# Performance work log

Hardware: AMD Instinct MI355X
Metric: run time of the kernel (lower is better)

## Reference

```python
import jax, jax.numpy as jnp
import numpy as np

N_GROUPS = 4
N_LIMITED_GROUPS = 2
TOP_K = 2
ROUTE_SCALE = 1.0


def setup_inputs() -> dict:
    key = jax.random.key(0)
    k1, k2, k3, k4 = jax.random.split(key, 4)
    n_tokens, dim, n_experts = 65536, 4096, 16
    return {
        "x": jax.random.normal(k1, (n_tokens, dim), dtype=jnp.float32),
        "w1_weight": jax.random.normal(k2, (n_experts, dim), dtype=jnp.float32) * 0.02,
        "w1_bias": jax.random.normal(k3, (n_experts,), dtype=jnp.float32) * 0.02,
        "route_bias": jax.random.normal(k4, (n_experts,), dtype=jnp.float32) * 0.02,
    }


def reference(x, w1_weight, w1_bias, route_bias):
    # Linear scorer: [N, E]
    logits = x @ w1_weight.T + w1_bias
    # softmax in fp32 (score_func == 'softmax')
    scores = jax.nn.softmax(logits.astype(jnp.float32), axis=-1)
    # bias add (moe_use_bias=True); original_scores includes the bias
    scores = scores + route_bias
    original_scores = scores

    n = x.shape[0]
    # group masking: view [N, n_groups, experts_per_group]
    g = scores.reshape(n, N_GROUPS, -1)
    group_scores = g.max(axis=-1)  # amax path since bias is not None
    _, gidx = jax.lax.top_k(group_scores, N_LIMITED_GROUPS)  # [N, n_limited]
    keep = jnp.zeros((n, N_GROUPS), dtype=bool).at[
        jnp.arange(n)[:, None], gidx
    ].set(True)
    masked = jnp.where(keep[:, :, None], g, -jnp.inf).reshape(n, -1)

    # top-k over masked scores; gather values from original (unmasked-at-topk) scores
    _, indices = jax.lax.top_k(masked, TOP_K)  # [N, k]
    values = jnp.take_along_axis(original_scores, indices, axis=1) * ROUTE_SCALE
    return values.astype(x.dtype), indices
```

## Files before the change

### kernel.cpp

```cpp
#include <hip/hip_runtime.h>
#include <math.h>

constexpr int NE = 16;
constexpr int NG = 4;
#define MARGIN 1e-4

typedef __attribute__((ext_vector_type(8))) short bf16x8;
typedef __attribute__((ext_vector_type(4))) float f32x4;

__device__ __forceinline__ unsigned short f2bf_rne(float f) {
    unsigned u = __float_as_uint(f);
    unsigned r = (u + 0x7fffu + ((u >> 16) & 1u)) >> 16;
    return (unsigned short)r;
}

__global__ __launch_bounds__(256)
void w_prep_kernel(const float* __restrict__ w, float* __restrict__ wt,
                   unsigned short* __restrict__ whi, unsigned short* __restrict__ wlo,
                   int dim, int n) {
    int id = blockIdx.x * 256 + threadIdx.x;
    if (id < n) {
        int e = id / dim;
        int k = id - e * dim;
        float f = w[id];
        wt[(size_t)k * NE + e] = f;
        unsigned short h = f2bf_rne(f);
        float back = __uint_as_float(((unsigned)h) << 16);
        whi[id] = h;
        wlo[id] = f2bf_rne(f - back);
    }
}

struct RouteR { double v1, v2; int i1, i2; double mg, mo, ms; };

__device__ __forceinline__ RouteR route_epilogue(const double* tot,
                                                 const float* w1b,
                                                 const float* rbias)
{
    double logit[NE];
    double m = -INFINITY;
#pragma unroll
    for (int e = 0; e < NE; ++e) {
        logit[e] = tot[e] + (double)w1b[e];
        m = fmax(m, logit[e]);
    }
    double ssum = 0.0, p[NE];
#pragma unroll
    for (int e = 0; e < NE; ++e) { p[e] = exp(logit[e] - m); ssum += p[e]; }
    double inv = 1.0 / ssum, sc[NE];
#pragma unroll
    for (int e = 0; e < NE; ++e) sc[e] = p[e] * inv + (double)rbias[e];

    double gm[NG];
#pragma unroll
    for (int g = 0; g < NG; ++g) {
        double a = fmax(sc[g * 4 + 0], sc[g * 4 + 1]);
        double b = fmax(sc[g * 4 + 2], sc[g * 4 + 3]);
        gm[g] = fmax(a, b);
    }
    int g1 = 0;
#pragma unroll
    for (int g = 1; g < NG; ++g) if (gm[g] > gm[g1]) g1 = g;
    int g2 = (g1 == 0) ? 1 : 0;
#pragma unroll
    for (int g = 0; g < NG; ++g) if (g != g1 && gm[g] > gm[g2]) g2 = g;
    double gm3 = -INFINITY;
#pragma unroll
    for (int g = 0; g < NG; ++g)
        if (g != g1 && g != g2 && gm[g] > gm3) gm3 = gm[g];

    RouteR r;
    r.v1 = -INFINITY; r.i1 = 0;
#pragma unroll
    for (int e = 0; e < NE; ++e) {
        int g = e >> 2;
        bool keep = (g == g1) || (g == g2);
        if (keep && sc[e] > r.v1) { r.v1 = sc[e]; r.i1 = e; }
    }
    r.v2 = -INFINITY; r.i2 = 0;
#pragma unroll
    for (int e = 0; e < NE; ++e) {
        int g = e >> 2;
        bool keep = ((g == g1) || (g == g2)) && (e != r.i1);
        if (keep && sc[e] > r.v2) { r.v2 = sc[e]; r.i2 = e; }
    }
    double v3 = -INFINITY;
#pragma unroll
    for (int e = 0; e < NE; ++e) {
        int g = e >> 2;
        bool keep = ((g == g1) || (g == g2)) && (e != r.i1) && (e != r.i2);
        if (keep && sc[e] > v3) v3 = sc[e];
    }
    r.mg = gm[g2] - gm3;
    r.mo = r.v1 - r.v2;
    r.ms = r.v2 - v3;
    return r;
}

__global__ __launch_bounds__(256)
void k1_mfma(const float* __restrict__ x,
             const unsigned short* __restrict__ whi,
             const unsigned short* __restrict__ wlo,
             const float* __restrict__ w1b,
             const float* __restrict__ rbias,
             float* __restrict__ dout,
             int* __restrict__ fcount,
             int* __restrict__ flist,
             int n_tokens, int dim)
{
    __shared__ float scl[4][16][NE + 1];
    const int tid  = threadIdx.x;
    const int wid  = tid >> 6;
    const int lane = tid & 63;
    const int m    = lane & 15;
    const int kg   = lane >> 4;
    const long tok0 = (long)blockIdx.x * 64 + wid * 16;
    const int nst = dim / 32;

    const float* xp = x + (tok0 + m) * (size_t)dim + kg * 8;
    const unsigned short* whp = whi + (size_t)m * dim + kg * 8;
    const unsigned short* wlp = wlo + (size_t)m * dim + kg * 8;

    f32x4 acc = {0.f, 0.f, 0.f, 0.f};

    float4 xa = *(const float4*)(xp);
    float4 xb = *(const float4*)(xp + 4);
    bf16x8 wh = *(const bf16x8*)(whp);
    bf16x8 wl = *(const bf16x8*)(wlp);

    for (int c = 0; c < nst; ++c) {
        float4 nxa = xa, nxb = xb;
        bf16x8 nwh = wh, nwl = wl;
        if (c + 1 < nst) {
            const float* xn = xp + (size_t)(c + 1) * 32;
            nxa = *(const float4*)(xn);
            nxb = *(const float4*)(xn + 4);
            nwh = *(const bf16x8*)(whp + (size_t)(c + 1) * 32);
            nwl = *(const bf16x8*)(wlp + (size_t)(c + 1) * 32);
        }

        float xf[8] = {xa.x, xa.y, xa.z, xa.w, xb.x, xb.y, xb.z, xb.w};
        bf16x8 xhi, xlo;
#pragma unroll
        for (int j = 0; j < 8; ++j) {
            float f = xf[j];
            unsigned short h = f2bf_rne(f);
            float back = __uint_as_float(((unsigned)h) << 16);
            xhi[j] = (short)h;
            xlo[j] = (short)f2bf_rne(f - back);
        }

        acc = __builtin_amdgcn_mfma_f32_16x16x32_bf16(xhi, wh, acc, 0, 0, 0);
        acc = __builtin_amdgcn_mfma_f32_16x16x32_bf16(xlo, wh, acc, 0, 0, 0);
        acc = __builtin_amdgcn_mfma_f32_16x16x32_bf16(xhi, wl, acc, 0, 0, 0);

        xa = nxa; xb = nxb; wh = nwh; wl = nwl;
    }

#pragma unroll
    for (int j = 0; j < 4; ++j)
        scl[wid][kg * 4 + j][m] = acc[j];

    if (lane < 16) {
        double tot[NE];
#pragma unroll
        for (int e = 0; e < NE; ++e) tot[e] = (double)scl[wid][lane][e];
        RouteR r = route_epilogue(tot, w1b, rbias);
        long tok = tok0 + lane;

        double mmin = fmin(r.mg, fmin(r.mo, r.ms));
        if (mmin < MARGIN) {
            int idx = atomicAdd(fcount, 1);
            if (idx < n_tokens) flist[idx] = (int)tok;
        }
        float2 vv; vv.x = (float)r.v1; vv.y = (float)r.v2;
        *(float2*)(dout + tok * 2) = vv;
        float2 iv; iv.x = (float)r.i1; iv.y = (float)r.i2;
        *(float2*)(dout + (long)n_tokens * 2 + tok * 2) = iv;
    }
}

__global__ __launch_bounds__(256)
void k2_recheck(const float* __restrict__ x,
                const float* __restrict__ wt,
                const float* __restrict__ w1b,
                const float* __restrict__ rbias,
                float* __restrict__ dout,
                const int* __restrict__ fcount,
                const int* __restrict__ flist,
                int n_tokens, int dim)
{
    const int tid  = threadIdx.x;
    const int lane = tid & 63;
    const int wavesPerBlock = blockDim.x >> 6;
    const int wglobal = blockIdx.x * wavesPerBlock + (tid >> 6);
    const int nwaves  = gridDim.x * wavesPerBlock;
    int nf = *fcount;
    if (nf > n_tokens) nf = n_tokens;
    const int nq = dim / 256;

    for (int i = wglobal; i < nf; i += nwaves) {
        const int t = flist[i];
        const float* xr = x + (size_t)t * dim;

        double part[NE];
#pragma unroll
        for (int e = 0; e < NE; ++e) part[e] = 0.0;

        for (int q = 0; q < nq; ++q) {
            float4 xv = *(const float4*)(xr + q * 256 + lane * 4);
#pragma unroll
            for (int j = 0; j < 4; ++j) {
                int k = q * 256 + lane * 4 + j;
                double xd = (double)((const float*)&xv)[j];
                const float* wr = wt + (size_t)k * NE;
#pragma unroll
                for (int e = 0; e < NE; ++e)
                    part[e] = fma(xd, (double)wr[e], part[e]);
            }
        }

#pragma unroll
        for (int off = 1; off < 64; off <<= 1) {
#pragma unroll
            for (int e = 0; e < NE; ++e)
                part[e] += __shfl_xor(part[e], off, 64);
        }

        RouteR r = route_epilogue(part, w1b, rbias);
        if (lane == 0) {
            float2 vv; vv.x = (float)r.v1; vv.y = (float)r.v2;
            *(float2*)(dout + (long)t * 2) = vv;
            float2 iv; iv.x = (float)r.i1; iv.y = (float)r.i2;
            *(float2*)(dout + (long)n_tokens * 2 + (long)t * 2) = iv;
        }
    }
}

__global__ __launch_bounds__(256)
void router_fallback(const float* __restrict__ x,
                     const float* __restrict__ w1w,
                     const float* __restrict__ w1b,
                     const float* __restrict__ rbias,
                     float* __restrict__ dout,
                     int n_tokens, int dim)
{
    __shared__ double wbuf4[4][16][NE];
    const int tid  = threadIdx.x;
    const int uwid = __builtin_amdgcn_readfirstlane(tid >> 6);
    const int lane = tid & 63;
    const int slice = dim / 4;
    const int nst  = slice / 16;
    const long tokA = (long)blockIdx.x * 128 + lane;
    const long tokB = tokA + 64;
    const float* xA = x + tokA * (size_t)dim + (size_t)uwid * slice;
    const float* xB = x + tokB * (size_t)dim + (size_t)uwid * slice;

    double accA[NE], accB[NE];
#pragma unroll
    for (int e = 0; e < NE; ++e) { accA[e] = 0.0; accB[e] = 0.0; }

    float4 a0 = *(const float4*)(xA + 0), a1 = *(const float4*)(xA + 4);
    float4 a2 = *(const float4*)(xA + 8), a3 = *(const float4*)(xA + 12);
    float4 b0 = *(const float4*)(xB + 0), b1 = *(const float4*)(xB + 4);
    float4 b2 = *(const float4*)(xB + 8), b3 = *(const float4*)(xB + 12);
    float4 wreg;
    {
        const int i0 = lane * 4;
#pragma unroll
        for (int j = 0; j < 4; ++j) {
            int i = i0 + j;
            ((float*)&wreg)[j] = w1w[(size_t)(i & 15) * dim + uwid * slice + (i >> 4)];
        }
    }

    for (int c = 0; c < nst; ++c) {
        {
            double* dst = &wbuf4[uwid][0][0] + lane * 4;
            dst[0] = (double)wreg.x;  dst[1] = (double)wreg.y;
            dst[2] = (double)wreg.z;  dst[3] = (double)wreg.w;
        }
        float4 na0=a0,na1=a1,na2=a2,na3=a3,nb0=b0,nb1=b1,nb2=b2,nb3=b3;
        if (c + 1 < nst) {
            const float* pa = xA + (c + 1) * 16;
            const float* pb = xB + (c + 1) * 16;
            na0 = *(const float4*)(pa + 0);  na1 = *(const float4*)(pa + 4);
            na2 = *(const float4*)(pa + 8);  na3 = *(const float4*)(pa + 12);
            nb0 = *(const float4*)(pb + 0);  nb1 = *(const float4*)(pb + 4);
            nb2 = *(const float4*)(pb + 8);  nb3 = *(const float4*)(pb + 12);
            const int kb = uwid * slice + (c + 1) * 16;
            const int i0 = lane * 4;
#pragma unroll
            for (int j = 0; j < 4; ++j) {
                int i = i0 + j;
                ((float*)&wreg)[j] = w1w[(size_t)(i & 15) * dim + kb + (i >> 4)];
            }
        }
        float fa[16], fb[16];
        fa[0]=a0.x; fa[1]=a0.y; fa[2]=a0.z; fa[3]=a0.w;
        fa[4]=a1.x; fa[5]=a1.y; fa[6]=a1.z; fa[7]=a1.w;
        fa[8]=a2.x; fa[9]=a2.y; fa[10]=a2.z; fa[11]=a2.w;
        fa[12]=a3.x; fa[13]=a3.y; fa[14]=a3.z; fa[15]=a3.w;
        fb[0]=b0.x; fb[1]=b0.y; fb[2]=b0.z; fb[3]=b0.w;
        fb[4]=b1.x; fb[5]=b1.y; fb[6]=b1.z; fb[7]=b1.w;
        fb[8]=b2.x; fb[9]=b2.y; fb[10]=b2.z; fb[11]=b2.w;
        fb[12]=b3.x; fb[13]=b3.y; fb[14]=b3.z; fb[15]=b3.w;
#pragma unroll
        for (int kk = 0; kk < 16; ++kk) {
            double xa_ = (double)fa[kk];
            double xb_ = (double)fb[kk];
#pragma unroll
            for (int ep = 0; ep < NE / 2; ++ep) {
                double2 wv = *(const double2*)&wbuf4[uwid][kk][ep * 2];
                accA[ep*2+0] = fma(xa_, wv.x, accA[ep*2+0]);
                accA[ep*2+1] = fma(xa_, wv.y, accA[ep*2+1]);
                accB[ep*2+0] = fma(xb_, wv.x, accB[ep*2+0]);
                accB[ep*2+1] = fma(xb_, wv.y, accB[ep*2+1]);
            }
        }
        a0=na0; a1=na1; a2=na2; a3=na3;
        b0=nb0; b1=nb1; b2=nb2; b3=nb3;
    }

    __syncthreads();
    __shared__ double red[3][2][64][NE + 1];
    if (uwid != 0) {
#pragma unroll
        for (int e = 0; e < NE; ++e) {
            red[uwid - 1][0][lane][e] = accA[e];
            red[uwid - 1][1][lane][e] = accB[e];
        }
    }
    __syncthreads();
    if (uwid != 0) return;

#pragma unroll
    for (int t = 0; t < 2; ++t) {
        double tot[NE];
#pragma unroll
        for (int e = 0; e < NE; ++e) {
            double a = (t == 0) ? accA[e] : accB[e];
            tot[e] = ((a + red[0][t][lane][e]) + red[1][t][lane][e])
                     + red[2][t][lane][e];
        }
        RouteR r = route_epilogue(tot, w1b, rbias);
        long tok = (t == 0) ? tokA : tokB;
        float2 vv; vv.x = (float)r.v1; vv.y = (float)r.v2;
        *(float2*)(dout + tok * 2) = vv;
        float2 iv; iv.x = (float)r.i1; iv.y = (float)r.i2;
        *(float2*)(dout + (long)n_tokens * 2 + tok * 2) = iv;
    }
}

extern "C" void kernel_launch(void* const* d_in, const int* in_sizes, int n_in,
                              void* d_out, int out_size, void* d_ws, size_t ws_size,
                              hipStream_t stream)
{
    const float* x   = (const float*)d_in[0];
    const float* w1w = (const float*)d_in[1];
    const float* w1b = (const float*)d_in[2];
    const float* rb  = (const float*)d_in[3];
    float* out = (float*)d_out;

    const int ne       = in_sizes[2];
    const int dim      = in_sizes[1] / ne;
    const int n_tokens = in_sizes[0] / dim;

    const int nW = dim * ne;
    const size_t WT_BYTES  = (size_t)nW * sizeof(float);
    const size_t WHI_OFF   = WT_BYTES;
    const size_t WLO_OFF   = WHI_OFF + (size_t)nW * 2;
    const size_t COUNT_OFF = WLO_OFF + (size_t)nW * 2;
    const size_t LIST_OFF  = COUNT_OFF + 128;
    const size_t need = LIST_OFF + (size_t)n_tokens * sizeof(int);

    if (ws_size >= need) {
        float* wt            = (float*)d_ws;
        unsigned short* whi  = (unsigned short*)((char*)d_ws + WHI_OFF);
        unsigned short* wlo  = (unsigned short*)((char*)d_ws + WLO_OFF);
        int* fcount          = (int*)((char*)d_ws + COUNT_OFF);
        int* flist           = (int*)((char*)d_ws + LIST_OFF);

        hipMemsetAsync(fcount, 0, sizeof(int), stream);
        hipLaunchKernelGGL(w_prep_kernel, dim3((nW + 255) / 256), dim3(256),
                           0, stream, w1w, wt, whi, wlo, dim, nW);
        hipLaunchKernelGGL(k1_mfma, dim3(n_tokens / 64), dim3(256),
                           0, stream, x, whi, wlo, w1b, rb, out, fcount, flist,
                           n_tokens, dim);
        hipLaunchKernelGGL(k2_recheck, dim3(256), dim3(256),
                           0, stream, x, wt, w1b, rb, out, fcount, flist,
                           n_tokens, dim);
    } else {
        hipLaunchKernelGGL(router_fallback, dim3(n_tokens / 128), dim3(256),
                           0, stream, x, w1w, w1b, rb, out, n_tokens, dim);
    }
}
```

Baseline: 323.2 us.

## Stage x tiles through LDS with async global_load_lds double buffering and split-K waves

The main scoring kernel now gives each block 16 tokens and splits the reduction dimension across its four waves. The x rows are streamed into a double-buffered LDS tile with direct global-to-LDS loads, guarded by explicit vmcnt waits and barriers. The four per-wave partial sums are added in the epilogue through LDS, in a fixed order and in double precision. The aim is fully coalesced, asynchronous loading of x that overlaps with the MFMA work. The cost is four times as many blocks, two block barriers per step, and wave 0 alone doing the routing epilogue.

```diff
diff --git a/kernel.cpp b/kernel.cpp
--- a/kernel.cpp
+++ b/kernel.cpp
@@ -12,6 +12,12 @@
     unsigned u = __float_as_uint(f);
     unsigned r = (u + 0x7fffu + ((u >> 16) & 1u)) >> 16;
     return (unsigned short)r;
+}
+
+__device__ __forceinline__ void gload_lds16(const float* g, float* l) {
+    __builtin_amdgcn_global_load_lds(
+        (const __attribute__((address_space(1))) void*)g,
+        (__attribute__((address_space(3))) void*)l, 16, 0, 0);
 }
 
 __global__ __launch_bounds__(256)
@@ -108,63 +114,95 @@
              int* __restrict__ flist,
              int n_tokens, int dim)
 {
-    __shared__ float scl[4][16][NE + 1];
+    __shared__ float tile[2][16][260];
     const int tid  = threadIdx.x;
-    const int wid  = tid >> 6;
+    const int uw   = __builtin_amdgcn_readfirstlane(tid >> 6);
     const int lane = tid & 63;
     const int m    = lane & 15;
     const int kg   = lane >> 4;
-    const long tok0 = (long)blockIdx.x * 64 + wid * 16;
-    const int nst = dim / 32;
-
-    const float* xp = x + (tok0 + m) * (size_t)dim + kg * 8;
-    const unsigned short* whp = whi + (size_t)m * dim + kg * 8;
-    const unsigned short* wlp = wlo + (size_t)m * dim + kg * 8;
+    const long tok0 = (long)blockIdx.x * 16;
+    const int nst = dim / 256;
+
+    const unsigned short* whp = whi + (size_t)m * dim + uw * 64 + kg * 8;
+    const unsigned short* wlp = wlo + (size_t)m * dim + uw * 64 + kg * 8;
 
     f32x4 acc = {0.f, 0.f, 0.f, 0.f};
 
-    float4 xa = *(const float4*)(xp);
-    float4 xb = *(const float4*)(xp + 4);
-    bf16x8 wh = *(const bf16x8*)(whp);
-    bf16x8 wl = *(const bf16x8*)(wlp);
-
-    for (int c = 0; c < nst; ++c) {
-        float4 nxa = xa, nxb = xb;
-        bf16x8 nwh = wh, nwl = wl;
-        if (c + 1 < nst) {
-            const float* xn = xp + (size_t)(c + 1) * 32;
-            nxa = *(const float4*)(xn);
-            nxb = *(const float4*)(xn + 4);
-            nwh = *(const bf16x8*)(whp + (size_t)(c + 1) * 32);
-            nwl = *(const bf16x8*)(wlp + (size_t)(c + 1) * 32);
-        }
-
-        float xf[8] = {xa.x, xa.y, xa.z, xa.w, xb.x, xb.y, xb.z, xb.w};
-        bf16x8 xhi, xlo;
-#pragma unroll
-        for (int j = 0; j < 8; ++j) {
-            float f = xf[j];
-            unsigned short h = f2bf_rne(f);
-            float back = __uint_as_float(((unsigned)h) << 16);
-            xhi[j] = (short)h;
-            xlo[j] = (short)f2bf_rne(f - back);
-        }
-
-        acc = __builtin_amdgcn_mfma_f32_16x16x32_bf16(xhi, wh, acc, 0, 0, 0);
-        acc = __builtin_amdgcn_mfma_f32_16x16x32_bf16(xlo, wh, acc, 0, 0, 0);
-        acc = __builtin_amdgcn_mfma_f32_16x16x32_bf16(xhi, wl, acc, 0, 0, 0);
-
-        xa = nxa; xb = nxb; wh = nwh; wl = nwl;
-    }
-
+    bf16x8 bh0 = *(const bf16x8*)(whp);
+    bf16x8 bh1 = *(const bf16x8*)(whp + 32);
+    bf16x8 bl0 = *(const bf16x8*)(wlp);
+    bf16x8 bl1 = *(const bf16x8*)(wlp + 32);
+#pragma unroll
+    for (int i = 0; i < 4; ++i)
+        gload_lds16(x + (tok0 + uw * 4 + i) * (size_t)dim + lane * 4,
+                    &tile[0][uw * 4 + i][0]);
+
+    int cur = 0;
+    for (int s = 0; s < nst; ++s) {
+        bf16x8 nbh0 = bh0, nbh1 = bh1, nbl0 = bl0, nbl1 = bl1;
+        if (s + 1 < nst) {
+            const unsigned short* wh2 = whp + (size_t)(s + 1) * 256;
+            const unsigned short* wl2 = wlp + (size_t)(s + 1) * 256;
+            nbh0 = *(const bf16x8*)(wh2);
+            nbh1 = *(const bf16x8*)(wh2 + 32);
+            nbl0 = *(const bf16x8*)(wl2);
+            nbl1 = *(const bf16x8*)(wl2 + 32);
+#pragma unroll
+            for (int i = 0; i < 4; ++i)
+                gload_lds16(x + (tok0 + uw * 4 + i) * (size_t)dim
+                              + (size_t)(s + 1) * 256 + lane * 4,
+                            &tile[cur ^ 1][uw * 4 + i][0]);
+            __builtin_amdgcn_sched_barrier(0);
+            asm volatile("s_waitcnt vmcnt(8)" ::: "memory");
+            __builtin_amdgcn_sched_barrier(0);
+        } else {
+            __builtin_amdgcn_sched_barrier(0);
+            asm volatile("s_waitcnt vmcnt(0)" ::: "memory");
+            __builtin_amdgcn_sched_barrier(0);
+        }
+        __builtin_amdgcn_s_barrier();
+        __builtin_amdgcn_sched_barrier(0);
+
+#pragma unroll
+        for (int it = 0; it < 2; ++it) {
+            const float* ap = &tile[cur][m][uw * 64 + kg * 8 + it * 32];
+            float4 xa = *(const float4*)ap;
+            float4 xb = *(const float4*)(ap + 4);
+            float xf[8] = {xa.x, xa.y, xa.z, xa.w, xb.x, xb.y, xb.z, xb.w};
+            bf16x8 xhi, xlo;
+#pragma unroll
+            for (int j = 0; j < 8; ++j) {
+                float f = xf[j];
+                unsigned short h = f2bf_rne(f);
+                float back = __uint_as_float(((unsigned)h) << 16);
+                xhi[j] = (short)h;
+                xlo[j] = (short)f2bf_rne(f - back);
+            }
+            bf16x8 wh = it ? bh1 : bh0;
+            bf16x8 wl = it ? bl1 : bl0;
+            acc = __builtin_amdgcn_mfma_f32_16x16x32_bf16(xhi, wh, acc, 0, 0, 0);
+            acc = __builtin_amdgcn_mfma_f32_16x16x32_bf16(xlo, wh, acc, 0, 0, 0);
+            acc = __builtin_amdgcn_mfma_f32_16x16x32_bf16(xhi, wl, acc, 0, 0, 0);
+        }
+        __builtin_amdgcn_sched_barrier(0);
+        __builtin_amdgcn_s_barrier();
+        __builtin_amdgcn_sched_barrier(0);
+        bh0 = nbh0; bh1 = nbh1; bl0 = nbl0; bl1 = nbl1;
+        cur ^= 1;
+    }
+
+    float (*red)[16][17] = (float (*)[16][17])(&tile[0][0][0]);
 #pragma unroll
     for (int j = 0; j < 4; ++j)
-        scl[wid][kg * 4 + j][m] = acc[j];
-
-    if (lane < 16) {
+        red[uw][kg * 4 + j][m] = acc[j];
+    __syncthreads();
+
+    if (uw == 0 && lane < 16) {
         double tot[NE];
 #pragma unroll
-        for (int e = 0; e < NE; ++e) tot[e] = (double)scl[wid][lane][e];
+        for (int e = 0; e < NE; ++e)
+            tot[e] = (((double)red[0][lane][e] + (double)red[1][lane][e])
+                      + (double)red[2][lane][e]) + (double)red[3][lane][e];
         RouteR r = route_epilogue(tot, w1b, rbias);
         long tok = tok0 + lane;
 
@@ -384,7 +422,7 @@
         hipMemsetAsync(fcount, 0, sizeof(int), stream);
         hipLaunchKernelGGL(w_prep_kernel, dim3((nW + 255) / 256), dim3(256),
                            0, stream, w1w, wt, whi, wlo, dim, nW);
-        hipLaunchKernelGGL(k1_mfma, dim3(n_tokens / 64), dim3(256),
+        hipLaunchKernelGGL(k1_mfma, dim3(n_tokens / 16), dim3(256),
                            0, stream, x, whi, wlo, w1b, rb, out, fcount, flist,
                            n_tokens, dim);
         hipLaunchKernelGGL(k2_recheck, dim3(256), dim3(256),
```

Result: faster. 271.0 us (median of 2 runs) (-16.1%).
